# Performance work log

Measured on AMD Instinct MI355X. Metric: run time of the kernel, lower is better.

Reference implementation:

```python
import jax, jax.numpy as jnp
import numpy as np

N_EXPERTS = 64
TOP_K = 2
DIM = 2048
N_TOKENS = 32768
SCALE = 1.0


def setup_inputs() -> dict:
    key = jax.random.key(0)
    k1, k2 = jax.random.split(key)
    x = jax.random.normal(k1, (N_TOKENS, DIM), dtype=jnp.float32)
    gate_w = jax.random.normal(k2, (N_EXPERTS, DIM), dtype=jnp.float32) * (1.0 / np.sqrt(DIM))
    return {"x": x, "gate_w": gate_w}


def reference(x, gate_w):
    # logits: (N, E) = x @ W^T, scaled
    logits = jnp.einsum("nd,ed->ne", x, gate_w) * SCALE
    topk_weights, expert_indices = jax.lax.top_k(logits, TOP_K)  # (N, k)
    topk_weights = jax.nn.softmax(topk_weights, axis=-1)
    # scatter ones at selected experts -> binary mask (N, E)
    expert_mask = jax.nn.one_hot(expert_indices, N_EXPERTS, dtype=logits.dtype).sum(axis=-2)
    return expert_mask, topk_weights, expert_indices
```

## Files before the change

### kernel.cpp

```cpp
#include <hip/hip_runtime.h>
#include <float.h>

#define NT 32768
#define DIM 2048
#define NE 64
#define TAU 1e-3f
#define CHUNK 128
#define NCH (DIM / CHUNK)

typedef __attribute__((ext_vector_type(8))) short short8;
typedef __attribute__((ext_vector_type(4))) float f32x4;

__device__ __forceinline__ unsigned short f2bf(float f) {
    unsigned u = __float_as_uint(f);
    u += 0x7fffu + ((u >> 16) & 1u);
    return (unsigned short)(u >> 16);
}
__device__ __forceinline__ float bf2f(unsigned short h) {
    return __uint_as_float(((unsigned)h) << 16);
}

__global__ __launch_bounds__(256)
void prep_w(const float* __restrict__ gw, unsigned short* __restrict__ wph,
            unsigned short* __restrict__ wpl, int* __restrict__ cnt) {
    const int gid  = blockIdx.x * 256 + threadIdx.x;
    const int lane = gid & 63;
    const int ksg  = (gid >> 6) & 63;
    const int et   = gid >> 12;
    const int e    = et * 16 + (lane & 15);
    const int k0   = ksg * 32 + (lane >> 4) * 8;

    float4 v0 = *(const float4*)(gw + (size_t)e * DIM + k0);
    float4 v1 = *(const float4*)(gw + (size_t)e * DIM + k0 + 4);
    float xf[8] = {v0.x, v0.y, v0.z, v0.w, v1.x, v1.y, v1.z, v1.w};
    short8 h, l;
#pragma unroll
    for (int j = 0; j < 8; ++j) {
        unsigned short hh = f2bf(xf[j]);
        h[j] = (short)hh;
        l[j] = (short)f2bf(xf[j] - bf2f(hh));
    }
    *(short8*)(wph + (size_t)gid * 8) = h;
    *(short8*)(wpl + (size_t)gid * 8) = l;
    if (gid == 0) *cnt = 0;
}

__global__ __launch_bounds__(256, 2)
void router_mfma(const float* __restrict__ x,
                 const unsigned short* __restrict__ wph,
                 const unsigned short* __restrict__ wpl,
                 float* __restrict__ out,
                 int* __restrict__ cnt, int* __restrict__ list) {
    __shared__ __align__(16) unsigned char smem[65536];

    const int tid  = threadIdx.x;
    const int lane = tid & 63;
    const int et   = tid >> 6;
    const int t0   = blockIdx.x * 64;

    const int sr = tid >> 4;
    const int sq = tid & 15;
    const unsigned swoff = (unsigned)((sr * 128 + sq * 8) ^ ((sr & 7) << 4));
    const float* xbase = x + (size_t)(t0 + sr) * DIM + sq * 4;

    const unsigned roff_e = (unsigned)((((lane & 15) * 128) | ((lane >> 4) << 4))
                                       ^ ((lane & 7) << 4));
    const unsigned roff_o = roff_e ^ 64u;

    f32x4 accP[4], accQ[4];
#pragma unroll
    for (int tt = 0; tt < 4; ++tt)
#pragma unroll
        for (int j = 0; j < 4; ++j) { accP[tt][j] = 0.f; accQ[tt][j] = 0.f; }

    float4 xrA[8], xrB[8];
    short8 Bh0[4], Bl0[4], Bh1[4], Bl1[4];

#define LOADX(bank_, c_) { _Pragma("unroll") for (int tt = 0; tt < 4; ++tt) \
    _Pragma("unroll") for (int i = 0; i < 2; ++i) \
        xr##bank_[tt*2+i] = *(const float4*)(xbase + (size_t)tt * 16 * DIM + (c_) * CHUNK + i * 64); }

#define BLOAD(bk_, c_) { _Pragma("unroll") for (int ksg = 0; ksg < 4; ++ksg) { \
        size_t o_ = (((size_t)et * 64 + ((c_) * 4 + ksg)) * 64 + lane) * 8; \
        Bh##bk_[ksg] = *(const short8*)(wph + o_); \
        Bl##bk_[ksg] = *(const short8*)(wpl + o_); } }

#define CVT_STORE(bank_, buf_) { _Pragma("unroll") for (int tt = 0; tt < 4; ++tt) \
    _Pragma("unroll") for (int i = 0; i < 2; ++i) { \
        float4 v_ = xr##bank_[tt*2+i]; \
        unsigned u0 = __float_as_uint(v_.x), u1 = __float_as_uint(v_.y); \
        unsigned u2 = __float_as_uint(v_.z), u3 = __float_as_uint(v_.w); \
        float l0 = v_.x - __uint_as_float(u0 & 0xffff0000u); \
        float l1 = v_.y - __uint_as_float(u1 & 0xffff0000u); \
        float l2 = v_.z - __uint_as_float(u2 & 0xffff0000u); \
        float l3 = v_.w - __uint_as_float(u3 & 0xffff0000u); \
        ushort4 hv_ = make_ushort4((unsigned short)(u0 >> 16), (unsigned short)(u1 >> 16), \
                                   (unsigned short)(u2 >> 16), (unsigned short)(u3 >> 16)); \
        ushort4 lv_ = make_ushort4((unsigned short)(__float_as_uint(l0) >> 16), \
                                   (unsigned short)(__float_as_uint(l1) >> 16), \
                                   (unsigned short)(__float_as_uint(l2) >> 16), \
                                   (unsigned short)(__float_as_uint(l3) >> 16)); \
        unsigned char* p_ = smem + (buf_) * 32768 + (tt*2+i) * 2048 + swoff; \
        *(ushort4*)p_ = hv_; \
        *(ushort4*)(p_ + 16384) = lv_; } }

#define MFMA_PHASE(buf_, bk_) { _Pragma("unroll") for (int ks = 0; ks < 4; ++ks) { \
        const unsigned ro_ = (ks & 1) ? roff_o : roff_e; \
        _Pragma("unroll") for (int tt = 0; tt < 4; ++tt) { \
            const unsigned char* pa_ = smem + (buf_) * 32768 + tt * 4096 + (ks >> 1) * 2048 + ro_; \
            short8 Ah_ = *(const short8*)pa_; \
            short8 Al_ = *(const short8*)(pa_ + 16384); \
            accP[tt] = __builtin_amdgcn_mfma_f32_16x16x32_bf16(Ah_, Bh##bk_[ks], accP[tt], 0, 0, 0); \
            accQ[tt] = __builtin_amdgcn_mfma_f32_16x16x32_bf16(Ah_, Bl##bk_[ks], accQ[tt], 0, 0, 0); \
            accQ[tt] = __builtin_amdgcn_mfma_f32_16x16x32_bf16(Al_, Bh##bk_[ks], accQ[tt], 0, 0, 0); } } }

#define BARSYNC { asm volatile("s_waitcnt lgkmcnt(0)" ::: "memory"); \
                  __builtin_amdgcn_sched_barrier(0); \
                  __builtin_amdgcn_s_barrier(); }

    LOADX(A, 0)
    LOADX(B, 1)
    BLOAD(0, 0)
    CVT_STORE(A, 0)
    BARSYNC

#pragma unroll 1
    for (int cc = 0; cc < 7; ++cc) {
        const int c0 = 2 * cc;
        LOADX(A, c0 + 2)
        BLOAD(1, c0 + 1)
        MFMA_PHASE(0, 0)
        CVT_STORE(B, 1)
        BARSYNC
        const int c1 = c0 + 1;
        LOADX(B, c1 + 2)
        BLOAD(0, c1 + 1)
        MFMA_PHASE(1, 1)
        CVT_STORE(A, 0)
        BARSYNC
    }
    BLOAD(1, 15)
    MFMA_PHASE(0, 0)
    CVT_STORE(B, 1)
    BARSYNC
    MFMA_PHASE(1, 1)

#undef LOADX
#undef BLOAD
#undef CVT_STORE
#undef MFMA_PHASE
#undef BARSYNC

    float* lmf = (float*)smem;
#pragma unroll
    for (int tt = 0; tt < 4; ++tt)
#pragma unroll
        for (int jr = 0; jr < 4; ++jr)
            lmf[(tt * 16 + (lane >> 4) * 4 + jr) * 68 + et * 16 + (lane & 15)] =
                accP[tt][jr] + accQ[tt][jr];
    __syncthreads();

    float* mout = out;
    float* wout = out + (size_t)NT * NE;
    float* iout = wout + (size_t)NT * 2;

    const int t   = tid >> 2;
    const int s   = tid & 3;
    const int tok = t0 + t;

    float vv[16];
#pragma unroll
    for (int j4 = 0; j4 < 4; ++j4) {
        float4 pv = *(const float4*)&lmf[t * 68 + s * 16 + j4 * 4];
        vv[j4 * 4] = pv.x; vv[j4 * 4 + 1] = pv.y; vv[j4 * 4 + 2] = pv.z; vv[j4 * 4 + 3] = pv.w;
    }

    float m1 = -FLT_MAX, m2 = -FLT_MAX, m3 = -FLT_MAX;
    int   i1 = NE, i2 = NE, i3 = NE;
    auto ins = [&](float v, int e) {
        bool b1 = (v > m1) || (v == m1 && e < i1);
        bool b2 = (v > m2) || (v == m2 && e < i2);
        bool b3 = (v > m3) || (v == m3 && e < i3);
        if (b1)      { m3 = m2; i3 = i2; m2 = m1; i2 = i1; m1 = v; i1 = e; }
        else if (b2) { m3 = m2; i3 = i2; m2 = v; i2 = e; }
        else if (b3) { m3 = v; i3 = e; }
    };
#pragma unroll
    for (int j = 0; j < 16; ++j) ins(vv[j], s * 16 + j);
#pragma unroll
    for (int off = 1; off <= 2; off <<= 1) {
        float om1 = __shfl_xor(m1, off, 64); int oi1 = __shfl_xor(i1, off, 64);
        float om2 = __shfl_xor(m2, off, 64); int oi2 = __shfl_xor(i2, off, 64);
        float om3 = __shfl_xor(m3, off, 64); int oi3 = __shfl_xor(i3, off, 64);
        ins(om1, oi1); ins(om2, oi2); ins(om3, oi3);
    }

    float ed  = expf(m2 - m1);
    float inv = 1.f / (1.f + ed);

#pragma unroll
    for (int j4 = 0; j4 < 4; ++j4) {
        float4 mv;
        int e0 = s * 16 + j4 * 4;
        mv.x = (e0     == i1 || e0     == i2) ? 1.f : 0.f;
        mv.y = (e0 + 1 == i1 || e0 + 1 == i2) ? 1.f : 0.f;
        mv.z = (e0 + 2 == i1 || e0 + 2 == i2) ? 1.f : 0.f;
        mv.w = (e0 + 3 == i1 || e0 + 3 == i2) ? 1.f : 0.f;
        *(float4*)(mout + (size_t)tok * NE + e0) = mv;
    }

    if (s == 0) {
        *(float2*)(wout + 2 * tok) = make_float2(inv, ed * inv);
        *(float2*)(iout + 2 * tok) = make_float2((float)i1, (float)i2);
        if ((m1 - m2 < TAU) || (m2 - m3 < TAU)) {
            int slot = atomicAdd(cnt, 1);
            list[slot] = tok;
        }
    }
}

__global__ __launch_bounds__(256)
void repair(const float* __restrict__ x, const float* __restrict__ gw,
            float* __restrict__ out, const int* __restrict__ cnt,
            const int* __restrict__ list) {
    __shared__ float red[64][5];
    const int n   = *cnt;
    const int tid = threadIdx.x;
    const int e   = tid & 63, qq = tid >> 6;

    float* mout = out;
    float* wout = out + (size_t)NT * NE;
    float* iout = wout + (size_t)NT * 2;

    for (int i = blockIdx.x; i < n; i += gridDim.x) {
        const int tok = list[i];
        const float* xr = x + (size_t)tok * DIM + qq * 512;
        const float* wr = gw + (size_t)e * DIM + qq * 512;
        float a = 0.f;
        for (int j = 0; j < 512; j += 4) {
            float4 xv = *(const float4*)(xr + j);
            float4 wv = *(const float4*)(wr + j);
            a = fmaf(xv.x, wv.x, a); a = fmaf(xv.y, wv.y, a);
            a = fmaf(xv.z, wv.z, a); a = fmaf(xv.w, wv.w, a);
        }
        red[e][qq] = a;
        __syncthreads();
        if (tid < 64) {
            float v = ((red[e][0] + red[e][1]) + red[e][2]) + red[e][3];
            float m1 = v, m2 = -FLT_MAX; int i1 = e, i2 = NE;
#pragma unroll
            for (int off = 1; off <= 32; off <<= 1) {
                float om1 = __shfl_xor(m1, off, 64); int oi1 = __shfl_xor(i1, off, 64);
                float om2 = __shfl_xor(m2, off, 64); int oi2 = __shfl_xor(i2, off, 64);
                bool selfFirst = (m1 > om1) || (m1 == om1 && i1 < oi1);
                if (selfFirst) {
                    if (!((m2 > om1) || (m2 == om1 && i2 < oi1))) { m2 = om1; i2 = oi1; }
                } else {
                    bool c = (m1 > om2) || (m1 == om2 && i1 < oi2);
                    if (c) { m2 = m1; i2 = i1; } else { m2 = om2; i2 = oi2; }
                    m1 = om1; i1 = oi1;
                }
            }
            float ed  = expf(m2 - m1);
            float inv = 1.f / (1.f + ed);
            mout[(size_t)tok * NE + e] = (e == i1 || e == i2) ? 1.f : 0.f;
            if (e == 0) {
                *(float2*)(wout + 2 * tok) = make_float2(inv, ed * inv);
                *(float2*)(iout + 2 * tok) = make_float2((float)i1, (float)i2);
            }
        }
        __syncthreads();
    }
}

extern "C" void kernel_launch(void* const* d_in, const int* in_sizes, int n_in,
                              void* d_out, int out_size, void* d_ws, size_t ws_size,
                              hipStream_t stream) {
    const float* x  = (const float*)d_in[0];
    const float* gw = (const float*)d_in[1];
    float* out = (float*)d_out;

    unsigned short* wph = (unsigned short*)d_ws;
    unsigned short* wpl = wph + (size_t)NE * DIM;
    int* cnt  = (int*)(wpl + (size_t)NE * DIM);
    int* list = cnt + 1;

    prep_w<<<dim3(64), dim3(256), 0, stream>>>(gw, wph, wpl, cnt);
    router_mfma<<<dim3(NT / 64), dim3(256), 0, stream>>>(x, wph, wpl, out, cnt, list);
    repair<<<dim3(256), dim3(256), 0, stream>>>(x, gw, out, cnt, list);
}
```

Baseline: 93.85 us.

## Halve K-chunk and LDS footprint to run four blocks per CU

Shrinks the per-iteration K chunk from 128 to 64 and the LDS buffer from 64KB to 32KB, raising the launch-bounds occupancy hint from 2 to 4 blocks per CU. The x staging is remapped so each thread loads 16 contiguous floats of one row, and the swizzled LDS addressing, B-fragment loads and double-buffer schedule are rewritten to match. The aim is to hide global-load latency through more resident waves instead of deep register prefetch. In exchange there are twice as many barrier-separated phases, a shallower software pipeline (the weight fragments are now loaded in the same phase that uses them), and a tighter register budget.

Result: slower. 113.0 us (+20.4%).

```diff
diff --git a/kernel.cpp b/kernel.cpp
--- a/kernel.cpp
+++ b/kernel.cpp
@@ -5,7 +5,7 @@
 #define DIM 2048
 #define NE 64
 #define TAU 1e-3f
-#define CHUNK 128
+#define CHUNK 64
 #define NCH (DIM / CHUNK)
 
 typedef __attribute__((ext_vector_type(8))) short short8;
@@ -45,27 +45,32 @@
     if (gid == 0) *cnt = 0;
 }
 
-__global__ __launch_bounds__(256, 2)
+__global__ __launch_bounds__(256, 4)
 void router_mfma(const float* __restrict__ x,
                  const unsigned short* __restrict__ wph,
                  const unsigned short* __restrict__ wpl,
                  float* __restrict__ out,
                  int* __restrict__ cnt, int* __restrict__ list) {
-    __shared__ __align__(16) unsigned char smem[65536];
+    __shared__ __align__(16) unsigned char smem[32768];
 
     const int tid  = threadIdx.x;
     const int lane = tid & 63;
     const int et   = tid >> 6;
     const int t0   = blockIdx.x * 64;
 
-    const int sr = tid >> 4;
-    const int sq = tid & 15;
-    const unsigned swoff = (unsigned)((sr * 128 + sq * 8) ^ ((sr & 7) << 4));
-    const float* xbase = x + (size_t)(t0 + sr) * DIM + sq * 4;
-
-    const unsigned roff_e = (unsigned)((((lane & 15) * 128) | ((lane >> 4) << 4))
-                                       ^ ((lane & 7) << 4));
-    const unsigned roff_o = roff_e ^ 64u;
+    const int srow = tid & 63;
+    const int so   = tid >> 6;
+    const unsigned sw0 = (unsigned)(srow * 128 + (((2 * so)     ^ (srow & 7)) << 4));
+    const unsigned sw1 = (unsigned)(srow * 128 + (((2 * so + 1) ^ (srow & 7)) << 4));
+    const float* xrow = x + (size_t)(t0 + srow) * DIM + so * 16;
+
+    unsigned rbase[4], koff[2];
+#pragma unroll
+    for (int tt = 0; tt < 4; ++tt)
+        rbase[tt] = (unsigned)((tt * 16 + (lane & 15)) * 128);
+#pragma unroll
+    for (int kg = 0; kg < 2; ++kg)
+        koff[kg] = (unsigned)(((kg * 4 + (lane >> 4)) ^ (lane & 7)) << 4);
 
     f32x4 accP[4], accQ[4];
 #pragma unroll
@@ -73,77 +78,73 @@
 #pragma unroll
         for (int j = 0; j < 4; ++j) { accP[tt][j] = 0.f; accQ[tt][j] = 0.f; }
 
-    float4 xrA[8], xrB[8];
-    short8 Bh0[4], Bl0[4], Bh1[4], Bl1[4];
-
-#define LOADX(bank_, c_) { _Pragma("unroll") for (int tt = 0; tt < 4; ++tt) \
-    _Pragma("unroll") for (int i = 0; i < 2; ++i) \
-        xr##bank_[tt*2+i] = *(const float4*)(xbase + (size_t)tt * 16 * DIM + (c_) * CHUNK + i * 64); }
-
-#define BLOAD(bk_, c_) { _Pragma("unroll") for (int ksg = 0; ksg < 4; ++ksg) { \
-        size_t o_ = (((size_t)et * 64 + ((c_) * 4 + ksg)) * 64 + lane) * 8; \
-        Bh##bk_[ksg] = *(const short8*)(wph + o_); \
-        Bl##bk_[ksg] = *(const short8*)(wpl + o_); } }
-
-#define CVT_STORE(bank_, buf_) { _Pragma("unroll") for (int tt = 0; tt < 4; ++tt) \
-    _Pragma("unroll") for (int i = 0; i < 2; ++i) { \
-        float4 v_ = xr##bank_[tt*2+i]; \
-        unsigned u0 = __float_as_uint(v_.x), u1 = __float_as_uint(v_.y); \
-        unsigned u2 = __float_as_uint(v_.z), u3 = __float_as_uint(v_.w); \
-        float l0 = v_.x - __uint_as_float(u0 & 0xffff0000u); \
-        float l1 = v_.y - __uint_as_float(u1 & 0xffff0000u); \
-        float l2 = v_.z - __uint_as_float(u2 & 0xffff0000u); \
-        float l3 = v_.w - __uint_as_float(u3 & 0xffff0000u); \
-        ushort4 hv_ = make_ushort4((unsigned short)(u0 >> 16), (unsigned short)(u1 >> 16), \
-                                   (unsigned short)(u2 >> 16), (unsigned short)(u3 >> 16)); \
-        ushort4 lv_ = make_ushort4((unsigned short)(__float_as_uint(l0) >> 16), \
-                                   (unsigned short)(__float_as_uint(l1) >> 16), \
-                                   (unsigned short)(__float_as_uint(l2) >> 16), \
-                                   (unsigned short)(__float_as_uint(l3) >> 16)); \
-        unsigned char* p_ = smem + (buf_) * 32768 + (tt*2+i) * 2048 + swoff; \
-        *(ushort4*)p_ = hv_; \
-        *(ushort4*)(p_ + 16384) = lv_; } }
-
-#define MFMA_PHASE(buf_, bk_) { _Pragma("unroll") for (int ks = 0; ks < 4; ++ks) { \
-        const unsigned ro_ = (ks & 1) ? roff_o : roff_e; \
-        _Pragma("unroll") for (int tt = 0; tt < 4; ++tt) { \
-            const unsigned char* pa_ = smem + (buf_) * 32768 + tt * 4096 + (ks >> 1) * 2048 + ro_; \
-            short8 Ah_ = *(const short8*)pa_; \
-            short8 Al_ = *(const short8*)(pa_ + 16384); \
-            accP[tt] = __builtin_amdgcn_mfma_f32_16x16x32_bf16(Ah_, Bh##bk_[ks], accP[tt], 0, 0, 0); \
-            accQ[tt] = __builtin_amdgcn_mfma_f32_16x16x32_bf16(Ah_, Bl##bk_[ks], accQ[tt], 0, 0, 0); \
-            accQ[tt] = __builtin_amdgcn_mfma_f32_16x16x32_bf16(Al_, Bh##bk_[ks], accQ[tt], 0, 0, 0); } } }
+    float4 xr[4];
+    short8 Bh[2], Bl[2];
+
+#define LOADX(c_) { _Pragma("unroll") for (int i = 0; i < 4; ++i) \
+        xr[i] = *(const float4*)(xrow + (c_) * CHUNK + i * 4); }
+
+#define BLOAD(c_) { _Pragma("unroll") for (int kg = 0; kg < 2; ++kg) { \
+        size_t o_ = (((size_t)et * 64 + ((c_) * 2 + kg)) * 64 + lane) * 8; \
+        Bh[kg] = *(const short8*)(wph + o_); \
+        Bl[kg] = *(const short8*)(wpl + o_); } }
+
+#define CVT_STORE(buf_) { \
+        _Pragma("unroll") for (int p = 0; p < 2; ++p) { \
+            float4 a_ = xr[2*p], b_ = xr[2*p+1]; \
+            float f_[8] = {a_.x, a_.y, a_.z, a_.w, b_.x, b_.y, b_.z, b_.w}; \
+            unsigned short hh[8], ll[8]; \
+            _Pragma("unroll") for (int j = 0; j < 8; ++j) { \
+                unsigned u_ = __float_as_uint(f_[j]); \
+                hh[j] = (unsigned short)(u_ >> 16); \
+                float lo_ = f_[j] - __uint_as_float(u_ & 0xffff0000u); \
+                ll[j] = (unsigned short)(__float_as_uint(lo_) >> 16); } \
+            unsigned char* p0_ = smem + (buf_) * 16384 + (p ? sw1 : sw0); \
+            *(ushort4*)p0_ = make_ushort4(hh[0], hh[1], hh[2], hh[3]); \
+            *(ushort4*)(p0_ + 8) = make_ushort4(hh[4], hh[5], hh[6], hh[7]); \
+            *(ushort4*)(p0_ + 8192) = make_ushort4(ll[0], ll[1], ll[2], ll[3]); \
+            *(ushort4*)(p0_ + 8200) = make_ushort4(ll[4], ll[5], ll[6], ll[7]); } }
+
+#define MFMA_PHASE(buf_) { _Pragma("unroll") for (int kg = 0; kg < 2; ++kg) \
+    _Pragma("unroll") for (int tt = 0; tt < 4; ++tt) { \
+        const unsigned char* pa_ = smem + (buf_) * 16384 + rbase[tt] + koff[kg]; \
+        short8 Ah_ = *(const short8*)pa_; \
+        short8 Al_ = *(const short8*)(pa_ + 8192); \
+        accP[tt] = __builtin_amdgcn_mfma_f32_16x16x32_bf16(Ah_, Bh[kg], accP[tt], 0, 0, 0); \
+        accQ[tt] = __builtin_amdgcn_mfma_f32_16x16x32_bf16(Ah_, Bl[kg], accQ[tt], 0, 0, 0); \
+        accQ[tt] = __builtin_amdgcn_mfma_f32_16x16x32_bf16(Al_, Bh[kg], accQ[tt], 0, 0, 0); } }
 
 #define BARSYNC { asm volatile("s_waitcnt lgkmcnt(0)" ::: "memory"); \
                   __builtin_amdgcn_sched_barrier(0); \
                   __builtin_amdgcn_s_barrier(); }
 
-    LOADX(A, 0)
-    LOADX(B, 1)
-    BLOAD(0, 0)
-    CVT_STORE(A, 0)
+    LOADX(0)
+    CVT_STORE(0)
     BARSYNC
 
 #pragma unroll 1
-    for (int cc = 0; cc < 7; ++cc) {
+    for (int cc = 0; cc < 15; ++cc) {
         const int c0 = 2 * cc;
-        LOADX(A, c0 + 2)
-        BLOAD(1, c0 + 1)
-        MFMA_PHASE(0, 0)
-        CVT_STORE(B, 1)
+        BLOAD(c0)
+        LOADX(c0 + 1)
+        MFMA_PHASE(0)
+        CVT_STORE(1)
         BARSYNC
         const int c1 = c0 + 1;
-        LOADX(B, c1 + 2)
-        BLOAD(0, c1 + 1)
-        MFMA_PHASE(1, 1)
-        CVT_STORE(A, 0)
+        BLOAD(c1)
+        LOADX(c1 + 1)
+        MFMA_PHASE(1)
+        CVT_STORE(0)
         BARSYNC
     }
-    BLOAD(1, 15)
-    MFMA_PHASE(0, 0)
-    CVT_STORE(B, 1)
+    BLOAD(30)
+    LOADX(31)
+    MFMA_PHASE(0)
+    CVT_STORE(1)
     BARSYNC
-    MFMA_PHASE(1, 1)
+    BLOAD(31)
+    MFMA_PHASE(1)
+    __syncthreads();
 
 #undef LOADX
 #undef BLOAD
```
